# Kernel optimization log

Hardware: AMD Instinct MI355X
Metric: run time of the kernel (lower is better)

## Reference

```python
import jax, jax.numpy as jnp
import numpy as np

N, M, D = 8192, 8192, 512

def setup_inputs() -> dict:
    key = jax.random.key(0)
    kx, ky = jax.random.split(key)
    x = jax.random.normal(kx, (N, D), dtype=jnp.float32)
    y = jax.random.normal(ky, (M, D), dtype=jnp.float32)
    gamma = jnp.ones((1,), dtype=jnp.float32)
    return {"x": x, "y": y, "gamma": gamma}

def reference(x, y, gamma):
    # Flatten leading dims as in the torch module
    x = x.reshape(-1, x.shape[-1])  # (N, D)
    y = y.reshape(-1, y.shape[-1])  # (M, D)
    x2 = jnp.sum(x * x, axis=-1)  # (N,)
    y2 = jnp.sum(y * y, axis=-1)  # (M,)
    xy = jnp.einsum('nd,md->nm', x, y)  # (N, M)
    sq_norm = x2[:, None] + y2[None, :] - 2.0 * xy
    return jnp.exp(-gamma[0] * sq_norm)
```

## Files before the change

### kernel.cpp

```cpp
#include <hip/hip_runtime.h>
#include <hip/hip_bf16.h>

#define NROWS 8192
#define DDIM  512
#define OUTN  8192

typedef short bf16x8 __attribute__((ext_vector_type(8)));
typedef float f32x4  __attribute__((ext_vector_type(4)));

__device__ __forceinline__ void gload_lds16(const void* g, void* l) {
    __builtin_amdgcn_global_load_lds(
        (const __attribute__((address_space(1))) void*)g,
        (__attribute__((address_space(3))) void*)l, 16, 0, 0);
}

__global__ void __launch_bounds__(256)
rbf_prep(const float* __restrict__ x, const float* __restrict__ y,
         unsigned short* __restrict__ xb, unsigned short* __restrict__ yb,
         float* __restrict__ x2, float* __restrict__ y2) {
    int wave = (blockIdx.x * blockDim.x + threadIdx.x) >> 6;
    int lane = threadIdx.x & 63;

    const float* src;
    unsigned short* dst;
    float* nrm;
    int row;
    if (wave < NROWS) { src = x; dst = xb; nrm = x2; row = wave; }
    else              { src = y; dst = yb; nrm = y2; row = wave - NROWS; }

    const float* p = src + (size_t)row * DDIM;
    unsigned short* q = dst + (size_t)row * DDIM;

    float s = 0.f;
#pragma unroll
    for (int it = 0; it < 4; ++it) {
        int idx = it * 128 + lane * 2;
        float2 v = *(const float2*)(p + idx);
        s += v.x * v.x + v.y * v.y;
        unsigned int ux = __float_as_uint(v.x);
        unsigned int uy = __float_as_uint(v.y);
        ux = (ux + 0x7fffu + ((ux >> 16) & 1u)) >> 16;
        uy = (uy + 0x7fffu + ((uy >> 16) & 1u)) >> 16;
        *(unsigned int*)(q + idx) = ux | (uy << 16);
    }
#pragma unroll
    for (int off = 32; off > 0; off >>= 1) s += __shfl_down(s, off, 64);
    if (lane == 0) nrm[row] = s;
}

__global__ void __launch_bounds__(256)
rbf_gemm(const unsigned short* __restrict__ xb,
         const unsigned short* __restrict__ yb,
         const float* __restrict__ x2, const float* __restrict__ y2,
         const float* __restrict__ gamma, float* __restrict__ out) {
    __shared__ unsigned short As[128 * 32];
    __shared__ unsigned short Bs[128 * 32];

    const int tid  = threadIdx.x;
    const int lane = tid & 63;
    const int w    = tid >> 6;
    const int wm   = w & 1;
    const int wn   = w >> 1;

    const int bm = blockIdx.x & 63;
    const int bn = blockIdx.x >> 6;
    const int row0 = bm * 128;
    const int col0 = bn * 128;

    f32x4 acc[4][4] = {};

    const int srow = lane >> 2;
    const int skc  = (lane & 3) * 8;

    for (int k0 = 0; k0 < DDIM; k0 += 32) {
#pragma unroll
        for (int i = 0; i < 2; ++i) {
            int rg = w * 32 + i * 16;
            const unsigned short* gp =
                xb + (size_t)(row0 + rg + srow) * DDIM + k0 + skc;
            gload_lds16(gp, As + rg * 32);
        }
#pragma unroll
        for (int i = 0; i < 2; ++i) {
            int rg = w * 32 + i * 16;
            const unsigned short* gp =
                yb + (size_t)(col0 + rg + srow) * DDIM + k0 + skc;
            gload_lds16(gp, Bs + rg * 32);
        }
        __syncthreads();

        bf16x8 af[4], bfr[4];
#pragma unroll
        for (int mi = 0; mi < 4; ++mi)
            af[mi] = *(const bf16x8*)(As + (wm * 64 + mi * 16 + (lane & 15)) * 32
                                         + (lane >> 4) * 8);
#pragma unroll
        for (int ni = 0; ni < 4; ++ni)
            bfr[ni] = *(const bf16x8*)(Bs + (wn * 64 + ni * 16 + (lane & 15)) * 32
                                          + (lane >> 4) * 8);
#pragma unroll
        for (int mi = 0; mi < 4; ++mi)
#pragma unroll
            for (int ni = 0; ni < 4; ++ni)
                acc[mi][ni] = __builtin_amdgcn_mfma_f32_16x16x32_bf16(
                    af[mi], bfr[ni], acc[mi][ni], 0, 0, 0);
        __syncthreads();
    }

    const float g = gamma[0];
#pragma unroll
    for (int mi = 0; mi < 4; ++mi) {
        const int rbase = row0 + wm * 64 + mi * 16 + (lane >> 4) * 4;
        float xn[4];
#pragma unroll
        for (int r = 0; r < 4; ++r) xn[r] = x2[rbase + r];
#pragma unroll
        for (int ni = 0; ni < 4; ++ni) {
            const int col = col0 + wn * 64 + ni * 16 + (lane & 15);
            const float yn = y2[col];
            float* op = out + (size_t)rbase * OUTN + col;
#pragma unroll
            for (int r = 0; r < 4; ++r) {
                float s = xn[r] + yn - 2.0f * acc[mi][ni][r];
                op[(size_t)r * OUTN] = __expf(-g * s);
            }
        }
    }
}

extern "C" void kernel_launch(void* const* d_in, const int* in_sizes, int n_in,
                              void* d_out, int out_size, void* d_ws, size_t ws_size,
                              hipStream_t stream) {
    const float* x     = (const float*)d_in[0];
    const float* y     = (const float*)d_in[1];
    const float* gamma = (const float*)d_in[2];
    float* out = (float*)d_out;

    char* ws = (char*)d_ws;
    unsigned short* xb = (unsigned short*)ws;
    unsigned short* yb = (unsigned short*)(ws + (size_t)NROWS * DDIM * 2);
    float* x2 = (float*)(ws + (size_t)NROWS * DDIM * 4);
    float* y2 = (float*)(ws + (size_t)NROWS * DDIM * 4 + NROWS * 4);

    rbf_prep<<<4096, 256, 0, stream>>>(x, y, xb, yb, x2, y2);

    rbf_gemm<<<4096, 256, 0, stream>>>(xb, yb, x2, y2, gamma, out);
}
```

Baseline: 349.7 us.

## Switch RBF GEMM from bf16 to fp8 scaled MFMA with swizzled LDS

The prep kernel now packs x and y to fp8 with packed-convert instructions instead of rounding to bf16. The GEMM uses the 16x16x128 f8f6f4 scaled MFMA with a K-tile of 128, loads 16-byte chunks into LDS under an XOR swizzle, and does four times fewer K iterations and barriers. The aim is to double matrix throughput and halve operand bytes. In exchange the x·y dot products are much less accurate, which could matter for inputs whose outputs are not saturated near zero.

```diff
diff --git a/kernel.cpp b/kernel.cpp
--- a/kernel.cpp
+++ b/kernel.cpp
@@ -1,12 +1,12 @@
 #include <hip/hip_runtime.h>
-#include <hip/hip_bf16.h>
 
 #define NROWS 8192
 #define DDIM  512
 #define OUTN  8192
 
-typedef short bf16x8 __attribute__((ext_vector_type(8)));
-typedef float f32x4  __attribute__((ext_vector_type(4)));
+typedef int   i32x4 __attribute__((ext_vector_type(4)));
+typedef int   i32x8 __attribute__((ext_vector_type(8)));
+typedef float f32x4 __attribute__((ext_vector_type(4)));
 
 __device__ __forceinline__ void gload_lds16(const void* g, void* l) {
     __builtin_amdgcn_global_load_lds(
@@ -16,45 +16,43 @@
 
 __global__ void __launch_bounds__(256)
 rbf_prep(const float* __restrict__ x, const float* __restrict__ y,
-         unsigned short* __restrict__ xb, unsigned short* __restrict__ yb,
+         unsigned char* __restrict__ xb, unsigned char* __restrict__ yb,
          float* __restrict__ x2, float* __restrict__ y2) {
     int wave = (blockIdx.x * blockDim.x + threadIdx.x) >> 6;
     int lane = threadIdx.x & 63;
 
     const float* src;
-    unsigned short* dst;
+    unsigned char* dst;
     float* nrm;
     int row;
     if (wave < NROWS) { src = x; dst = xb; nrm = x2; row = wave; }
     else              { src = y; dst = yb; nrm = y2; row = wave - NROWS; }
 
-    const float* p = src + (size_t)row * DDIM;
-    unsigned short* q = dst + (size_t)row * DDIM;
+    const float* p = src + (size_t)row * DDIM + lane * 8;
+    float4 v0 = *(const float4*)(p);
+    float4 v1 = *(const float4*)(p + 4);
 
-    float s = 0.f;
-#pragma unroll
-    for (int it = 0; it < 4; ++it) {
-        int idx = it * 128 + lane * 2;
-        float2 v = *(const float2*)(p + idx);
-        s += v.x * v.x + v.y * v.y;
-        unsigned int ux = __float_as_uint(v.x);
-        unsigned int uy = __float_as_uint(v.y);
-        ux = (ux + 0x7fffu + ((ux >> 16) & 1u)) >> 16;
-        uy = (uy + 0x7fffu + ((uy >> 16) & 1u)) >> 16;
-        *(unsigned int*)(q + idx) = ux | (uy << 16);
-    }
+    float s = v0.x * v0.x + v0.y * v0.y + v0.z * v0.z + v0.w * v0.w
+            + v1.x * v1.x + v1.y * v1.y + v1.z * v1.z + v1.w * v1.w;
+
+    int lo = __builtin_amdgcn_cvt_pk_fp8_f32(v0.x, v0.y, 0, false);
+    lo     = __builtin_amdgcn_cvt_pk_fp8_f32(v0.z, v0.w, lo, true);
+    int hi = __builtin_amdgcn_cvt_pk_fp8_f32(v1.x, v1.y, 0, false);
+    hi     = __builtin_amdgcn_cvt_pk_fp8_f32(v1.z, v1.w, hi, true);
+    *(int2*)(dst + (size_t)row * DDIM + lane * 8) = make_int2(lo, hi);
+
 #pragma unroll
     for (int off = 32; off > 0; off >>= 1) s += __shfl_down(s, off, 64);
     if (lane == 0) nrm[row] = s;
 }
 
 __global__ void __launch_bounds__(256)
-rbf_gemm(const unsigned short* __restrict__ xb,
-         const unsigned short* __restrict__ yb,
+rbf_gemm(const unsigned char* __restrict__ xb,
+         const unsigned char* __restrict__ yb,
          const float* __restrict__ x2, const float* __restrict__ y2,
          const float* __restrict__ gamma, float* __restrict__ out) {
-    __shared__ unsigned short As[128 * 32];
-    __shared__ unsigned short Bs[128 * 32];
+    __shared__ unsigned char As[128 * 128];
+    __shared__ unsigned char Bs[128 * 128];
 
     const int tid  = threadIdx.x;
     const int lane = tid & 63;
@@ -69,41 +67,46 @@
 
     f32x4 acc[4][4] = {};
 
-    const int srow = lane >> 2;
-    const int skc  = (lane & 3) * 8;
+    const int srl = lane >> 3;
+    const int sgc = ((lane & 7) ^ srl) * 16;
 
-    for (int k0 = 0; k0 < DDIM; k0 += 32) {
+    for (int k0 = 0; k0 < DDIM; k0 += 128) {
 #pragma unroll
-        for (int i = 0; i < 2; ++i) {
-            int rg = w * 32 + i * 16;
-            const unsigned short* gp =
-                xb + (size_t)(row0 + rg + srow) * DDIM + k0 + skc;
-            gload_lds16(gp, As + rg * 32);
-        }
-#pragma unroll
-        for (int i = 0; i < 2; ++i) {
-            int rg = w * 32 + i * 16;
-            const unsigned short* gp =
-                yb + (size_t)(col0 + rg + srow) * DDIM + k0 + skc;
-            gload_lds16(gp, Bs + rg * 32);
+        for (int i = 0; i < 4; ++i) {
+            int rg = w * 32 + i * 8;
+            gload_lds16(xb + (size_t)(row0 + rg + srl) * DDIM + k0 + sgc,
+                        As + rg * 128);
+            gload_lds16(yb + (size_t)(col0 + rg + srl) * DDIM + k0 + sgc,
+                        Bs + rg * 128);
         }
         __syncthreads();
 
-        bf16x8 af[4], bfr[4];
+        const int sw = lane & 7;
+        const int g2 = (lane >> 4) * 2;
+        i32x8 af[4], bfr[4];
 #pragma unroll
-        for (int mi = 0; mi < 4; ++mi)
-            af[mi] = *(const bf16x8*)(As + (wm * 64 + mi * 16 + (lane & 15)) * 32
-                                         + (lane >> 4) * 8);
+        for (int mi = 0; mi < 4; ++mi) {
+            const unsigned char* base = As + (wm * 64 + mi * 16 + (lane & 15)) * 128;
+            i32x4 lo = *(const i32x4*)(base + ((g2    ) ^ sw) * 16);
+            i32x4 hi = *(const i32x4*)(base + ((g2 + 1) ^ sw) * 16);
+            af[mi] = __builtin_shufflevector(lo, hi, 0, 1, 2, 3, 4, 5, 6, 7);
+        }
 #pragma unroll
-        for (int ni = 0; ni < 4; ++ni)
-            bfr[ni] = *(const bf16x8*)(Bs + (wn * 64 + ni * 16 + (lane & 15)) * 32
-                                          + (lane >> 4) * 8);
+        for (int ni = 0; ni < 4; ++ni) {
+            const unsigned char* base = Bs + (wn * 64 + ni * 16 + (lane & 15)) * 128;
+            i32x4 lo = *(const i32x4*)(base + ((g2    ) ^ sw) * 16);
+            i32x4 hi = *(const i32x4*)(base + ((g2 + 1) ^ sw) * 16);
+            bfr[ni] = __builtin_shufflevector(lo, hi, 0, 1, 2, 3, 4, 5, 6, 7);
+        }
 #pragma unroll
         for (int mi = 0; mi < 4; ++mi)
 #pragma unroll
             for (int ni = 0; ni < 4; ++ni)
-                acc[mi][ni] = __builtin_amdgcn_mfma_f32_16x16x32_bf16(
-                    af[mi], bfr[ni], acc[mi][ni], 0, 0, 0);
+                acc[mi][ni] = __builtin_amdgcn_mfma_scale_f32_16x16x128_f8f6f4(
+                    af[mi], bfr[ni], acc[mi][ni],
+                    0, 0,
+                    0, 0x7F,
+                    0, 0x7F);
         __syncthreads();
     }
 
@@ -137,12 +140,11 @@
     float* out = (float*)d_out;
 
     char* ws = (char*)d_ws;
-    unsigned short* xb = (unsigned short*)ws;
-    unsigned short* yb = (unsigned short*)(ws + (size_t)NROWS * DDIM * 2);
-    float* x2 = (float*)(ws + (size_t)NROWS * DDIM * 4);
-    float* y2 = (float*)(ws + (size_t)NROWS * DDIM * 4 + NROWS * 4);
+    unsigned char* xb = (unsigned char*)ws;
+    unsigned char* yb = (unsigned char*)(ws + (size_t)NROWS * DDIM);
+    float* x2 = (float*)(ws + (size_t)NROWS * DDIM * 2);
+    float* y2 = (float*)(ws + (size_t)NROWS * DDIM * 2 + NROWS * 4);
 
     rbf_prep<<<4096, 256, 0, stream>>>(x, y, xb, yb, x2, y2);
-
     rbf_gemm<<<4096, 256, 0, stream>>>(xb, yb, x2, y2, gamma, out);
 }
```

After: 323.4 us. -7.5%, faster.
